# Optimization experiments

Hardware: AMD Instinct MI355X
Metric: run time of the kernel (lower is better)

Reference implementation:

```python
import jax, jax.numpy as jnp
import numpy as np

N = 50000
E = 600000
D = 128
H = 8
DH = D // H
SCALE = float(np.sqrt(DH))


def setup_inputs() -> dict:
    key = jax.random.key(0)
    ks = jax.random.split(key, 12)
    s = 1.0 / np.sqrt(D)
    return {
        "x": jax.random.normal(ks[0], (N, D), jnp.float32),
        "edge_index": jax.random.randint(ks[1], (2, E), 0, N, jnp.int64),
        "edge_attr": jax.random.normal(ks[2], (E,), jnp.float32),
        "Wq": jax.random.uniform(ks[3], (D, D), jnp.float32, -s, s),
        "bq": jax.random.uniform(ks[4], (D,), jnp.float32, -s, s),
        "Wk": jax.random.uniform(ks[5], (D, D), jnp.float32, -s, s),
        "bk": jax.random.uniform(ks[6], (D,), jnp.float32, -s, s),
        "Wv": jax.random.uniform(ks[7], (D, D), jnp.float32, -s, s),
        "bv": jax.random.uniform(ks[8], (D,), jnp.float32, -s, s),
        "Wo": jax.random.uniform(ks[9], (D, D), jnp.float32, -s, s),
        "bo": jax.random.uniform(ks[10], (D,), jnp.float32, -s, s),
    }


def reference(x, edge_index, edge_attr, Wq, bq, Wk, bk, Wv, bv, Wo, bo):
    # Projections -> [N, H, DH]
    Q = (x @ Wq + bq).reshape(N, H, DH)
    K = (x @ Wk + bk).reshape(N, H, DH)
    V = (x @ Wv + bv).reshape(N, H, DH)
    row, col = edge_index[0], edge_index[1]
    q_i = Q[row]   # [E, H, DH] gather by destination (source of softmax segment)
    k_j = K[col]
    v_j = V[col]
    scores = jnp.sum(q_i * k_j, axis=-1) / SCALE  # [E, H]
    scores = scores + edge_attr[:, None]          # edge_attr broadcast over heads
    # Segment softmax per row-node; max is taken over heads then per node (as original)
    edge_max = scores.max(axis=1)                                  # [E]
    node_max = jax.ops.segment_max(edge_max, row, num_segments=N)  # [N]
    s_exp = jnp.exp(scores - node_max[row][:, None])               # [E, H]
    s_sum = jax.ops.segment_sum(s_exp, row, num_segments=N)        # [N, H]
    attn = s_exp / (s_sum[row] + 1e-8)                             # [E, H]
    # (dropout is identity in eval mode)
    out = jax.ops.segment_sum(attn[:, :, None] * v_j, row, num_segments=N)  # [N, H, DH]
    out = out.reshape(N, D)
    return out @ Wo + bo
```

## Files before the change

kernel.cpp:

```cpp
#include <hip/hip_runtime.h>
#include <math.h>

#define N_NODES 50000
#define N_EDGES 600000
#define DIM 128
#define HEADS 8
#define NBLK 196
#define EBLK 2344
#define HBLK 586
#define GBLK 1563

typedef _Float16 v8h __attribute__((ext_vector_type(8)));
typedef _Float16 v2h __attribute__((ext_vector_type(2)));
typedef float v16f __attribute__((ext_vector_type(16)));
typedef float v2f __attribute__((ext_vector_type(2)));

union v8h_u {
    v8h v;
    v2h p[4];
    _Float16 e[8];
};

__device__ __forceinline__ float e4m3_to_f32_sw(unsigned int b) {
    unsigned int s = b >> 7, E = (b >> 3) & 0xF, m = b & 7;
    float v = (E == 0) ? (float)m * 0.001953125f
                       : ldexpf(1.0f + (float)m * 0.125f, (int)E - 7);
    return s ? -v : v;
}

template <bool HI>
__device__ __forceinline__ v2f cvt2_f8(unsigned int w) {
#if __has_builtin(__builtin_amdgcn_cvt_pk_f32_fp8)
    return __builtin_amdgcn_cvt_pk_f32_fp8((int)w, HI);
#else
    v2f r;
    r[0] = e4m3_to_f32_sw((w >> (HI ? 16 : 0)) & 0xff);
    r[1] = e4m3_to_f32_sw((w >> (HI ? 24 : 8)) & 0xff);
    return r;
#endif
}

__device__ __forceinline__ unsigned char f32_to_e4m3(float v) {
#if __has_builtin(__builtin_amdgcn_cvt_pk_fp8_f32)
    return (unsigned char)(__builtin_amdgcn_cvt_pk_fp8_f32(v, v, 0, false) & 0xff);
#else
    float a = fabsf(v);
    unsigned char sgn = (v < 0.f) ? 0x80 : 0;
    if (!(a >= 0.0078125f)) {
        int m = (int)(a * 512.0f + 0.5f);
        if (m > 7) return sgn | 8;
        return sgn | (unsigned char)m;
    }
    if (a >= 448.0f) return sgn | 0x7e;
    int e;
    float fr = frexpf(a, &e);
    int mant = (int)(fr * 16.0f + 0.5f);
    int E = e + 6;
    if (mant == 16) { mant = 8; E++; }
    if (E >= 16) return sgn | 0x7e;
    return sgn | (unsigned char)((E << 3) | (mant - 8));
#endif
}

__global__ __launch_bounds__(256) void prep_kernel(const float* __restrict__ Wq,
                                                   const float* __restrict__ Wk,
                                                   const float* __restrict__ Wv,
                                                   const float* __restrict__ Wo,
                                                   _Float16* __restrict__ Wfrag,
                                                   int* __restrict__ counts,
                                                   int* __restrict__ cursor) {
    int i = blockIdx.x * 256 + threadIdx.x;
    if (i < N_NODES) counts[i] = 0;
    if (i == 0) cursor[0] = 0;
    if (i < 16384) {
        int base = i * 4;
        int mat = i >> 12;
        int rem = i & 4095;
        int wave = rem >> 10;
        int kt = (rem >> 7) & 7;
        int lane = (rem >> 1) & 63;
        int jh = (rem & 1) * 4;
        const float* src = (mat == 0) ? Wq : (mat == 1) ? Wk : (mat == 2) ? Wv : Wo;
        int n = wave * 32 + (lane & 31);
        int kbase = kt * 16 + (lane >> 5) * 8 + jh;
        _Float16 o[4];
#pragma unroll
        for (int j = 0; j < 4; j++) o[j] = (_Float16)src[(kbase + j) * 128 + n];
        *(short4*)(Wfrag + base) = *(short4*)o;
    }
}

#define LDSTRIDE 132
__global__ __launch_bounds__(256) void qkv_hist(const float* __restrict__ x,
                                                const _Float16* __restrict__ Wfrag,
                                                const float* __restrict__ bq,
                                                const float* __restrict__ bk,
                                                const float* __restrict__ bv,
                                                _Float16* __restrict__ Qh,
                                                unsigned char* __restrict__ K8,
                                                _Float16* __restrict__ Vh,
                                                const int* __restrict__ rowi,
                                                int* __restrict__ counts,
                                                int* __restrict__ rank) {
    __shared__ _Float16 As[32 * LDSTRIDE];
    if (blockIdx.x >= GBLK) {
        int e0 = (blockIdx.x - GBLK) * 1024 + threadIdx.x;
        int r[4], rk[4];
#pragma unroll
        for (int k = 0; k < 4; k++) {
            int e = e0 + k * 256;
            r[k] = (e < N_EDGES) ? rowi[e] : -1;
        }
#pragma unroll
        for (int k = 0; k < 4; k++)
            if (r[k] >= 0) rk[k] = atomicAdd(counts + r[k], 1);
#pragma unroll
        for (int k = 0; k < 4; k++) {
            int e = e0 + k * 256;
            if (e < N_EDGES) rank[e] = rk[k];
        }
        return;
    }
    int tid = threadIdx.x;
    int wave = tid >> 6, lane = tid & 63;
    int m32 = lane & 31, quad = lane >> 5;
    int row0 = blockIdx.x * 32;

    {
        int r = tid >> 3;
        int c0 = (tid & 7) * 16;
        int gr = row0 + r;
        bool valid = gr < N_NODES;
        const float4* src = (const float4*)(x + (size_t)gr * 128 + c0);
        _Float16* dst = As + r * LDSTRIDE + c0;
#pragma unroll
        for (int q = 0; q < 4; q++) {
            float4 v = valid ? src[q] : make_float4(0.f, 0.f, 0.f, 0.f);
            _Float16 o[4] = {(_Float16)v.x, (_Float16)v.y, (_Float16)v.z, (_Float16)v.w};
            *(short4*)(dst + q * 4) = *(short4*)o;
        }
    }
    __syncthreads();

    v8h af[8];
#pragma unroll
    for (int kt = 0; kt < 8; kt++)
        af[kt] = *(const v8h*)(As + m32 * LDSTRIDE + kt * 16 + quad * 8);

    int col = wave * 32 + m32;
#pragma unroll
    for (int mat = 0; mat < 3; mat++) {
        const _Float16* wf = Wfrag + mat * 16384 + wave * 4096 + lane * 8;
        v16f acc;
#pragma unroll
        for (int r = 0; r < 16; r++) acc[r] = 0.0f;
#pragma unroll
        for (int kt = 0; kt < 8; kt++) {
            v8h bf = *(const v8h*)(wf + kt * 512);
            acc = __builtin_amdgcn_mfma_f32_32x32x16_f16(af[kt], bf, acc, 0, 0, 0);
        }
        const float* bias = (mat == 0) ? bq : (mat == 1) ? bk : bv;
        float bias_v = bias[col];
        if (mat == 1) {
#pragma unroll
            for (int r = 0; r < 16; r++) {
                int row = (r & 3) + 8 * (r >> 2) + 4 * quad;
                int gr = row0 + row;
                if (gr < N_NODES) K8[(size_t)gr * 128 + col] = f32_to_e4m3(acc[r] + bias_v);
            }
        } else {
            _Float16* C = (mat == 0) ? Qh : Vh;
#pragma unroll
            for (int r = 0; r < 16; r++) {
                int row = (r & 3) + 8 * (r >> 2) + 4 * quad;
                int gr = row0 + row;
                if (gr < N_NODES) C[(size_t)gr * 128 + col] = (_Float16)(acc[r] + bias_v);
            }
        }
    }
}

__global__ __launch_bounds__(256) void alloc_scan(const int* __restrict__ counts,
                                                  int* __restrict__ start,
                                                  int* __restrict__ cursor) {
    __shared__ int sh[256];
    __shared__ int base;
    int t = threadIdx.x;
    int idx = blockIdx.x * 256 + t;
    int v = (idx < N_NODES) ? counts[idx] : 0;
    sh[t] = v;
    __syncthreads();
    for (int off = 1; off < 256; off <<= 1) {
        int a = sh[t];
        int b = (t >= off) ? sh[t - off] : 0;
        __syncthreads();
        sh[t] = a + b;
        __syncthreads();
    }
    if (t == 255) base = atomicAdd(cursor, sh[255]);
    __syncthreads();
    if (idx < N_NODES) start[idx] = base + sh[t] - v;
}

__global__ __launch_bounds__(256) void scatter_k(const int* __restrict__ rowi,
                                                 const int* __restrict__ coli,
                                                 const float* __restrict__ eattr,
                                                 const int* __restrict__ start,
                                                 const int* __restrict__ rank,
                                                 unsigned int* __restrict__ ep4) {
    int e = blockIdx.x * 256 + threadIdx.x;
    if (e >= N_EDGES) return;
    int pos = start[rowi[e]] + rank[e];
    unsigned short eb = __builtin_bit_cast(unsigned short, (_Float16)eattr[e]);
    ep4[pos] = (unsigned int)coli[e] | ((unsigned int)eb << 16);
}

__global__ __launch_bounds__(256) void gemm_out(const _Float16* __restrict__ Ah,
                                                const _Float16* __restrict__ Wfrag,
                                                const float* __restrict__ bo,
                                                float* __restrict__ C) {
    __shared__ _Float16 As[32 * LDSTRIDE];
    int tid = threadIdx.x;
    int wave = tid >> 6, lane = tid & 63;
    int m32 = lane & 31, quad = lane >> 5;
    int row0 = blockIdx.x * 32;

    {
        int r = tid >> 3;
        int c0 = (tid & 7) * 16;
        int gr = row0 + r;
        bool valid = gr < N_NODES;
        const v8h* src = (const v8h*)(Ah + (size_t)gr * 128 + c0);
        _Float16* dst = As + r * LDSTRIDE + c0;
        v8h z = {};
        *(v8h*)(dst) = valid ? src[0] : z;
        *(v8h*)(dst + 8) = valid ? src[1] : z;
    }
    __syncthreads();

    v8h af[8];
#pragma unroll
    for (int kt = 0; kt < 8; kt++)
        af[kt] = *(const v8h*)(As + m32 * LDSTRIDE + kt * 16 + quad * 8);

    int col = wave * 32 + m32;
    const _Float16* wf = Wfrag + 3 * 16384 + wave * 4096 + lane * 8;
    v16f acc;
#pragma unroll
    for (int r = 0; r < 16; r++) acc[r] = 0.0f;
#pragma unroll
    for (int kt = 0; kt < 8; kt++) {
        v8h bf = *(const v8h*)(wf + kt * 512);
        acc = __builtin_amdgcn_mfma_f32_32x32x16_f16(af[kt], bf, acc, 0, 0, 0);
    }
    float bias_v = bo[col];
#pragma unroll
    for (int r = 0; r < 16; r++) {
        int row = (r & 3) + 8 * (r >> 2) + 4 * quad;
        int gr = row0 + row;
        if (gr < N_NODES) C[(size_t)gr * 128 + col] = acc[r] + bias_v;
    }
}

__global__ __launch_bounds__(256) void fused_attn(const _Float16* __restrict__ Q,
                                                  const unsigned char* __restrict__ K8,
                                                  const _Float16* __restrict__ V,
                                                  const int* __restrict__ start,
                                                  const int* __restrict__ counts,
                                                  const unsigned int* __restrict__ ep4,
                                                  _Float16* __restrict__ Aout) {
    int t = blockIdx.x * 256 + threadIdx.x;
    int n = t >> 4;
    int sub = t & 15;
    if (n >= N_NODES) return;

    int s0 = start[n];
    int cnt = counts[n];
    int e1 = s0 + cnt;

    v8h_u q;
    q.v = *(const v8h*)(Q + (size_t)n * 128 + sub * 8);
    float qf[8];
#pragma unroll
    for (int j = 0; j < 8; j++) qf[j] = (float)q.e[j];

    const unsigned char* Kb = K8 + sub * 8;
    const _Float16* Vb = V + sub * 8;

    float l = 0.0f;
    float acc[8];
#pragma unroll
    for (int j = 0; j < 8; j++) acc[j] = 0.0f;

    int nb = (cnt + 15) >> 4;
    for (int b = 0; b < nb; b++) {
        int base = s0 + (b << 4);
        int li = base + sub;
        if (li >= e1) li = e1 - 1;
        unsigned int pv = ep4[li];

#pragma unroll
        for (int h = 0; h < 2; h++) {
            int hb = h << 3;
            if (base + hb < e1) {
                int cols[8];
                float eas[8];
#pragma unroll
                for (int u = 0; u < 8; u++) {
                    unsigned int w = (unsigned int)__shfl((int)pv, hb + u, 16);
                    cols[u] = (int)(w & 0xffffu);
                    eas[u] = (float)__builtin_bit_cast(_Float16, (unsigned short)(w >> 16));
                }
                uint2 kw[8];
                v8h_u vv[8];
#pragma unroll
                for (int u = 0; u < 8; u++) {
                    kw[u] = *(const uint2*)(Kb + ((size_t)cols[u] << 7));
                    vv[u].v = *(const v8h*)(Vb + ((size_t)cols[u] << 7));
                }
                __builtin_amdgcn_sched_barrier(0);
#pragma unroll
                for (int u = 0; u < 8; u++) {
                    v2f k01 = cvt2_f8<false>(kw[u].x);
                    v2f k23 = cvt2_f8<true>(kw[u].x);
                    v2f k45 = cvt2_f8<false>(kw[u].y);
                    v2f k67 = cvt2_f8<true>(kw[u].y);
                    float dot = 0.0f;
                    dot = fmaf(qf[0], k01[0], dot);
                    dot = fmaf(qf[1], k01[1], dot);
                    dot = fmaf(qf[2], k23[0], dot);
                    dot = fmaf(qf[3], k23[1], dot);
                    dot = fmaf(qf[4], k45[0], dot);
                    dot = fmaf(qf[5], k45[1], dot);
                    dot = fmaf(qf[6], k67[0], dot);
                    dot = fmaf(qf[7], k67[1], dot);
                    dot += __shfl_xor(dot, 1);
                    float s = dot * 0.25f + eas[u];
                    bool valid = (base + hb + u) < e1;
                    float ex = valid ? __expf(s) : 0.0f;
                    l += ex;
#pragma unroll
                    for (int j = 0; j < 8; j++) acc[j] = fmaf(ex, (float)vv[u].e[j], acc[j]);
                }
            }
        }
    }

    float inv = 1.0f / (l + 1e-8f);
    _Float16 tmp[8];
#pragma unroll
    for (int j = 0; j < 8; j++) tmp[j] = (_Float16)(acc[j] * inv);
    *(v8h*)(Aout + (size_t)n * 128 + sub * 8) = *(v8h*)tmp;
}

extern "C" void kernel_launch(void* const* d_in, const int* in_sizes, int n_in,
                              void* d_out, int out_size, void* d_ws, size_t ws_size,
                              hipStream_t stream) {
    const float* x = (const float*)d_in[0];
    const int* ei = (const int*)d_in[1];
    const float* eattr = (const float*)d_in[2];
    const float* Wq = (const float*)d_in[3];
    const float* bq = (const float*)d_in[4];
    const float* Wk = (const float*)d_in[5];
    const float* bk = (const float*)d_in[6];
    const float* Wv = (const float*)d_in[7];
    const float* bv = (const float*)d_in[8];
    const float* Wo = (const float*)d_in[9];
    const float* bo = (const float*)d_in[10];
    float* out = (float*)d_out;

    const int* rowi = ei;
    const int* coli = ei + N_EDGES;

    _Float16* Qh = (_Float16*)d_ws;
    _Float16* Vh = Qh + (size_t)N_NODES * DIM;
    _Float16* Ah = Vh + (size_t)N_NODES * DIM;
    unsigned char* K8 = (unsigned char*)(Ah + (size_t)N_NODES * DIM);
    _Float16* Wfrag = (_Float16*)(K8 + (size_t)N_NODES * DIM);
    int* counts = (int*)(Wfrag + 4 * 16384);
    int* start = counts + N_NODES;
    int* rank = start + N_NODES;
    int* cursor = rank + N_EDGES;
    unsigned int* ep4 = (unsigned int*)(cursor + 2);

    prep_kernel<<<NBLK, 256, 0, stream>>>(Wq, Wk, Wv, Wo, Wfrag, counts, cursor);
    qkv_hist<<<GBLK + HBLK, 256, 0, stream>>>(x, Wfrag, bq, bk, bv, Qh, K8, Vh,
                                              rowi, counts, rank);
    alloc_scan<<<NBLK, 256, 0, stream>>>(counts, start, cursor);
    scatter_k<<<EBLK, 256, 0, stream>>>(rowi, coli, eattr, start, rank, ep4);
    int ablocks = (N_NODES * 16 + 255) / 256;
    fused_attn<<<ablocks, 256, 0, stream>>>(Qh, K8, Vh, start, counts, ep4, Ah);
    gemm_out<<<GBLK, 256, 0, stream>>>(Ah, Wfrag, bo, out);
}
```

Measured before the change: 191.5 us.

## Replace global-atomic CSR build with two-level LDS radix bucketing of edges

Edges are now bucketed into CSR order by a two-pass radix sort instead of per-edge global atomics on node counts followed by a rank scatter. Pass one bins edges by the high bits of the row (256-node buckets) using LDS histograms and block-level scans. Pass two sorts each bucket by its low 8 bits inside LDS and writes counts, start and the packed edge records. The aim is to remove heavily contended global atomics and random scattered writes, at the cost of more kernel launches and an extra pass over 8-byte intermediate records. Ordering within a node is no longer the original edge order, which only changes floating-point summation order.

Result: faster. 177.0 us (-7.6%).

```diff
diff --git a/kernel.cpp b/kernel.cpp
--- a/kernel.cpp
+++ b/kernel.cpp
@@ -5,10 +5,10 @@
 #define N_EDGES 600000
 #define DIM 128
 #define HEADS 8
-#define NBLK 196
 #define EBLK 2344
-#define HBLK 586
 #define GBLK 1563
+#define NB1 586
+#define L1E 1024
 
 typedef _Float16 v8h __attribute__((ext_vector_type(8)));
 typedef _Float16 v2h __attribute__((ext_vector_type(2)));
@@ -66,12 +66,8 @@
                                                    const float* __restrict__ Wk,
                                                    const float* __restrict__ Wv,
                                                    const float* __restrict__ Wo,
-                                                   _Float16* __restrict__ Wfrag,
-                                                   int* __restrict__ counts,
-                                                   int* __restrict__ cursor) {
+                                                   _Float16* __restrict__ Wfrag) {
     int i = blockIdx.x * 256 + threadIdx.x;
-    if (i < N_NODES) counts[i] = 0;
-    if (i == 0) cursor[0] = 0;
     if (i < 16384) {
         int base = i * 4;
         int mat = i >> 12;
@@ -100,25 +96,22 @@
                                                 unsigned char* __restrict__ K8,
                                                 _Float16* __restrict__ Vh,
                                                 const int* __restrict__ rowi,
-                                                int* __restrict__ counts,
-                                                int* __restrict__ rank) {
+                                                int* __restrict__ bh) {
     __shared__ _Float16 As[32 * LDSTRIDE];
+    __shared__ int lh[256];
     if (blockIdx.x >= GBLK) {
-        int e0 = (blockIdx.x - GBLK) * 1024 + threadIdx.x;
-        int r[4], rk[4];
+        int b = blockIdx.x - GBLK;
+        int t = threadIdx.x;
+        lh[t] = 0;
+        __syncthreads();
+        int e0 = b * L1E + t;
 #pragma unroll
         for (int k = 0; k < 4; k++) {
             int e = e0 + k * 256;
-            r[k] = (e < N_EDGES) ? rowi[e] : -1;
-        }
-#pragma unroll
-        for (int k = 0; k < 4; k++)
-            if (r[k] >= 0) rk[k] = atomicAdd(counts + r[k], 1);
-#pragma unroll
-        for (int k = 0; k < 4; k++) {
-            int e = e0 + k * 256;
-            if (e < N_EDGES) rank[e] = rk[k];
-        }
+            if (e < N_EDGES) atomicAdd(lh + (rowi[e] >> 8), 1);
+        }
+        __syncthreads();
+        bh[t * NB1 + b] = lh[t];
         return;
     }
     int tid = threadIdx.x;
@@ -180,39 +173,114 @@
     }
 }
 
-__global__ __launch_bounds__(256) void alloc_scan(const int* __restrict__ counts,
-                                                  int* __restrict__ start,
-                                                  int* __restrict__ cursor) {
+__global__ __launch_bounds__(256) void scanA(const int* __restrict__ bh,
+                                             int* __restrict__ within,
+                                             int* __restrict__ dt) {
     __shared__ int sh[256];
-    __shared__ int base;
+    int d = blockIdx.x, t = threadIdx.x;
+    int carry = 0;
+    for (int c = 0; c < 3; c++) {
+        int j = c * 256 + t;
+        int v = (j < NB1) ? bh[d * NB1 + j] : 0;
+        __syncthreads();
+        sh[t] = v;
+        __syncthreads();
+        for (int off = 1; off < 256; off <<= 1) {
+            int a = sh[t];
+            int b2 = (t >= off) ? sh[t - off] : 0;
+            __syncthreads();
+            sh[t] = a + b2;
+            __syncthreads();
+        }
+        if (j < NB1) within[d * NB1 + j] = carry + sh[t] - v;
+        carry += sh[255];
+    }
+    if (t == 0) dt[d] = carry;
+}
+
+__global__ __launch_bounds__(256) void scanB(const int* __restrict__ dt,
+                                             int* __restrict__ dto) {
+    __shared__ int sh[256];
     int t = threadIdx.x;
-    int idx = blockIdx.x * 256 + t;
-    int v = (idx < N_NODES) ? counts[idx] : 0;
+    int v = dt[t];
     sh[t] = v;
     __syncthreads();
     for (int off = 1; off < 256; off <<= 1) {
         int a = sh[t];
-        int b = (t >= off) ? sh[t - off] : 0;
-        __syncthreads();
-        sh[t] = a + b;
-        __syncthreads();
-    }
-    if (t == 255) base = atomicAdd(cursor, sh[255]);
-    __syncthreads();
-    if (idx < N_NODES) start[idx] = base + sh[t] - v;
-}
-
-__global__ __launch_bounds__(256) void scatter_k(const int* __restrict__ rowi,
-                                                 const int* __restrict__ coli,
-                                                 const float* __restrict__ eattr,
-                                                 const int* __restrict__ start,
-                                                 const int* __restrict__ rank,
-                                                 unsigned int* __restrict__ ep4) {
-    int e = blockIdx.x * 256 + threadIdx.x;
-    if (e >= N_EDGES) return;
-    int pos = start[rowi[e]] + rank[e];
-    unsigned short eb = __builtin_bit_cast(unsigned short, (_Float16)eattr[e]);
-    ep4[pos] = (unsigned int)coli[e] | ((unsigned int)eb << 16);
+        int b2 = (t >= off) ? sh[t - off] : 0;
+        __syncthreads();
+        sh[t] = a + b2;
+        __syncthreads();
+    }
+    dto[t] = sh[t] - v;
+}
+
+__global__ __launch_bounds__(256) void l1scat(const int* __restrict__ rowi,
+                                              const int* __restrict__ coli,
+                                              const float* __restrict__ eattr,
+                                              const int* __restrict__ within,
+                                              const int* __restrict__ dto,
+                                              unsigned long long* __restrict__ rec1) {
+    __shared__ int lh[256], base[256];
+    int b = blockIdx.x, t = threadIdx.x;
+    lh[t] = 0;
+    base[t] = dto[t] + within[t * NB1 + b];
+    __syncthreads();
+    int e0 = b * L1E + t;
+#pragma unroll
+    for (int k = 0; k < 4; k++) {
+        int e = e0 + k * 256;
+        if (e < N_EDGES) {
+            int row = rowi[e];
+            int d = row >> 8;
+            int r = atomicAdd(lh + d, 1);
+            unsigned short eb = __builtin_bit_cast(unsigned short, (_Float16)eattr[e]);
+            rec1[base[d] + r] = (unsigned long long)row |
+                                ((unsigned long long)(unsigned int)coli[e] << 16) |
+                                ((unsigned long long)eb << 32);
+        }
+    }
+}
+
+__global__ __launch_bounds__(256) void l2sort(const unsigned long long* __restrict__ rec1,
+                                              const int* __restrict__ dto,
+                                              const int* __restrict__ dt,
+                                              int* __restrict__ counts,
+                                              int* __restrict__ start,
+                                              unsigned int* __restrict__ ep4) {
+    __shared__ int h[256], hs[256], r2[256], sh[256];
+    int d = blockIdx.x, t = threadIdx.x;
+    int s = dto[d], cnt = dt[d];
+    int e = s + cnt;
+    h[t] = 0;
+    r2[t] = 0;
+    __syncthreads();
+    for (int i = s + t; i < e; i += 256) atomicAdd(h + (int)(rec1[i] & 255), 1);
+    __syncthreads();
+    int v = h[t];
+    sh[t] = v;
+    __syncthreads();
+    for (int off = 1; off < 256; off <<= 1) {
+        int a = sh[t];
+        int b2 = (t >= off) ? sh[t - off] : 0;
+        __syncthreads();
+        sh[t] = a + b2;
+        __syncthreads();
+    }
+    int ex = sh[t] - v;
+    hs[t] = ex;
+    int node = (d << 8) | t;
+    if (node < N_NODES) {
+        counts[node] = v;
+        start[node] = s + ex;
+    }
+    __syncthreads();
+    for (int i = s + t; i < e; i += 256) {
+        unsigned long long w = rec1[i];
+        int ld = (int)(w & 255);
+        int r = atomicAdd(r2 + ld, 1);
+        ep4[s + hs[ld] + r] = (unsigned int)(w >> 16);
+    }
 }
 
 __global__ __launch_bounds__(256) void gemm_out(const _Float16* __restrict__ Ah,
@@ -379,15 +447,20 @@
     _Float16* Wfrag = (_Float16*)(K8 + (size_t)N_NODES * DIM);
     int* counts = (int*)(Wfrag + 4 * 16384);
     int* start = counts + N_NODES;
-    int* rank = start + N_NODES;
-    int* cursor = rank + N_EDGES;
-    unsigned int* ep4 = (unsigned int*)(cursor + 2);
-
-    prep_kernel<<<NBLK, 256, 0, stream>>>(Wq, Wk, Wv, Wo, Wfrag, counts, cursor);
-    qkv_hist<<<GBLK + HBLK, 256, 0, stream>>>(x, Wfrag, bq, bk, bv, Qh, K8, Vh,
-                                              rowi, counts, rank);
-    alloc_scan<<<NBLK, 256, 0, stream>>>(counts, start, cursor);
-    scatter_k<<<EBLK, 256, 0, stream>>>(rowi, coli, eattr, start, rank, ep4);
+    int* bh = start + N_NODES;
+    int* within = bh + 256 * NB1;
+    int* dt = within + 256 * NB1;
+    int* dto = dt + 256;
+    unsigned long long* rec1 = (unsigned long long*)(dto + 256);
+    unsigned int* ep4 = (unsigned int*)(rec1 + N_EDGES);
+
+    prep_kernel<<<64, 256, 0, stream>>>(Wq, Wk, Wv, Wo, Wfrag);
+    qkv_hist<<<GBLK + NB1, 256, 0, stream>>>(x, Wfrag, bq, bk, bv, Qh, K8, Vh,
+                                             rowi, bh);
+    scanA<<<256, 256, 0, stream>>>(bh, within, dt);
+    scanB<<<1, 256, 0, stream>>>(dt, dto);
+    l1scat<<<NB1, 256, 0, stream>>>(rowi, coli, eattr, within, dto, rec1);
+    l2sort<<<196, 256, 0, stream>>>(rec1, dto, dt, counts, start, ep4);
     int ablocks = (N_NODES * 16 + 255) / 256;
     fused_attn<<<ablocks, 256, 0, stream>>>(Qh, K8, Vh, start, counts, ep4, Ah);
     gemm_out<<<GBLK, 256, 0, stream>>>(Ah, Wfrag, bo, out);
```
